# Kernel optimization log

Measured on AMD Instinct MI355X. Metric: run time of the kernel, lower is better.

The kernel has to match this reference:

```python
import jax, jax.numpy as jnp
import numpy as np

N_NODES = 100000
N_EDGES = 625000
IN_DIM = 128
NUM_CLASSES = 2


def setup_inputs() -> dict:
    key = jax.random.key(0)
    k1, k2, k3 = jax.random.split(key, 3)
    x = jax.random.normal(k1, (N_NODES, IN_DIM), dtype=jnp.float32)
    edge_index = jax.random.randint(k2, (2, N_EDGES), 0, N_NODES, dtype=jnp.int64)
    # nn.Linear(2*in_dim, num_classes): weight [out, in], bias [out]
    W = jax.random.normal(k3, (NUM_CLASSES, 2 * IN_DIM), dtype=jnp.float32) * (1.0 / np.sqrt(2 * IN_DIM))
    b = jnp.zeros((NUM_CLASSES,), dtype=jnp.float32)
    return {"x": x, "edge_index": edge_index, "W": W, "b": b}


def reference(x, edge_index, W, b):
    # Gather src/dst node features per edge, concat, linear classifier.
    src, dst = edge_index[0], edge_index[1]
    h = jnp.concatenate([x[src], x[dst]], axis=-1)  # [E, 2*in_dim]
    score = jnp.einsum('ed,cd->ec', h, W) + b        # [E, num_classes]
    return score
```

## Files before the change

### kernel.cpp

```cpp
#include <hip/hip_runtime.h>
#include <hip/hip_bf16.h>

#define IN_DIM 128

__global__ __launch_bounds__(256) void node_proj_kernel(
    const float* __restrict__ x,
    const float* __restrict__ W,
    float4* __restrict__ p,
    int n_nodes) {
    __shared__ __align__(16) float wlds[4 * 144];

    for (int i = threadIdx.x; i < 512; i += 256) {
        int c    = i >> 8;
        int d    = i & 255;
        int half = d >> 7;
        int k    = d & 127;
        int sub  = k >> 5;
        int kk   = k & 31;
        wlds[(half * 2 + c) * 144 + sub * 36 + kk] = W[i];
    }
    __syncthreads();

    const int lane = threadIdx.x & 63;
    const int sub  = lane & 3;
    const int nl   = lane >> 2;
    const int wave = threadIdx.x >> 6;
    const int node = (blockIdx.x * 4 + wave) * 16 + nl;

    if (node < n_nodes) {
        const float* xb = x + (size_t)node * IN_DIM + sub * 32;
        const float* wt = wlds + sub * 36;

        float a0 = 0.f, a1 = 0.f, d0 = 0.f, d1 = 0.f;
        #pragma unroll
        for (int j = 0; j < 8; ++j) {
            const float4 xv = *(const float4*)(xb + j * 4);
            const float4 w0 = *(const float4*)(wt + 0 * 144 + j * 4);
            const float4 w1 = *(const float4*)(wt + 1 * 144 + j * 4);
            const float4 w2 = *(const float4*)(wt + 2 * 144 + j * 4);
            const float4 w3 = *(const float4*)(wt + 3 * 144 + j * 4);
            a0 += xv.x * w0.x + xv.y * w0.y + xv.z * w0.z + xv.w * w0.w;
            a1 += xv.x * w1.x + xv.y * w1.y + xv.z * w1.z + xv.w * w1.w;
            d0 += xv.x * w2.x + xv.y * w2.y + xv.z * w2.z + xv.w * w2.w;
            d1 += xv.x * w3.x + xv.y * w3.y + xv.z * w3.z + xv.w * w3.w;
        }

        a0 += __shfl_xor(a0, 1, 64);
        a1 += __shfl_xor(a1, 1, 64);
        d0 += __shfl_xor(d0, 1, 64);
        d1 += __shfl_xor(d1, 1, 64);
        a0 += __shfl_xor(a0, 2, 64);
        a1 += __shfl_xor(a1, 2, 64);
        d0 += __shfl_xor(d0, 2, 64);
        d1 += __shfl_xor(d1, 2, 64);

        if (sub == 0) {
            p[node] = make_float4(a0, a1, d0, d1);
        }
    }
}

__global__ __launch_bounds__(256) void edge_score_kernel(
    const int* __restrict__ idx,
    const float4* __restrict__ p,
    const float* __restrict__ b,
    float2* __restrict__ out,
    int n_edges) {
    const int e = blockIdx.x * blockDim.x + threadIdx.x;
    if (e >= n_edges) return;
    const int s = idx[e];
    const int d = idx[n_edges + e];
    const float4 ps = p[s];
    const float4 pd = p[d];
    const float b0 = b[0];
    const float b1 = b[1];
    float2 o;
    o.x = ps.x + pd.z + b0;
    o.y = ps.y + pd.w + b1;
    out[e] = o;
}

extern "C" void kernel_launch(void* const* d_in, const int* in_sizes, int n_in,
                              void* d_out, int out_size, void* d_ws, size_t ws_size,
                              hipStream_t stream) {
    const float* x   = (const float*)d_in[0];
    const int*   idx = (const int*)d_in[1];
    const float* W   = (const float*)d_in[2];
    const float* b   = (const float*)d_in[3];
    float* out = (float*)d_out;

    const int n_nodes = in_sizes[0] / IN_DIM;
    const int n_edges = in_sizes[1] / 2;

    float4* p = (float4*)d_ws;

    const int blocks1 = (n_nodes + 63) / 64;
    node_proj_kernel<<<blocks1, 256, 0, stream>>>(x, W, p, n_nodes);

    const int blocks2 = (n_edges + 255) / 256;
    edge_score_kernel<<<blocks2, 256, 0, stream>>>(idx, p, b, (float2*)out, n_edges);
}
```

Measured before the change: 101.2 us.

## Fuse node projection and edge scoring into one persistent kernel with grid barrier

Merges the node-projection and edge-scoring kernels into a single persistent kernel of 256 blocks. Blocks synchronise through an atomic-counter grid barrier instead of a second launch. Edge indices are prefetched into registers before the projection phase so their load overlaps the node work. The projections are split into separate src/dst float2 arrays so each edge gather reads 8 bytes per endpoint instead of 16, and edges are handled four at a time with vectorised index loads and output stores. In exchange it adds a memset launch and a spin barrier that assumes all 256 blocks are co-resident, and it uses a fixed grid that may underfill the GPU.

```diff
diff --git a/kernel.cpp b/kernel.cpp
--- a/kernel.cpp
+++ b/kernel.cpp
@@ -2,15 +2,23 @@
 #include <hip/hip_bf16.h>
 
 #define IN_DIM 128
+#define NBLK 256
+#define NTHR 256
+#define MAX_GRP 3
 
-__global__ __launch_bounds__(256) void node_proj_kernel(
+__global__ __launch_bounds__(NTHR, 2) void fused_predictor_kernel(
     const float* __restrict__ x,
+    const int*   __restrict__ idx,
     const float* __restrict__ W,
-    float4* __restrict__ p,
-    int n_nodes) {
+    const float* __restrict__ b,
+    float*       __restrict__ out,
+    float2*      __restrict__ pa,
+    float2*      __restrict__ pd,
+    unsigned int* __restrict__ counter,
+    int n_nodes, int n_edges) {
     __shared__ __align__(16) float wlds[4 * 144];
 
-    for (int i = threadIdx.x; i < 512; i += 256) {
+    for (int i = threadIdx.x; i < 512; i += NTHR) {
         int c    = i >> 8;
         int d    = i & 255;
         int half = d >> 7;
@@ -19,65 +27,104 @@
         int kk   = k & 31;
         wlds[(half * 2 + c) * 144 + sub * 36 + kk] = W[i];
     }
+
+    const int tglob    = blockIdx.x * NTHR + threadIdx.x;
+    const int n_groups = n_edges >> 2;
+    int4 sg[MAX_GRP], dg[MAX_GRP];
+    #pragma unroll
+    for (int i = 0; i < MAX_GRP; ++i) {
+        int g = tglob + i * (NBLK * NTHR);
+        if (g < n_groups) {
+            sg[i] = *(const int4*)(idx + 4 * g);
+            dg[i] = *(const int4*)(idx + n_edges + 4 * g);
+        }
+    }
+    const float b0 = b[0];
+    const float b1 = b[1];
     __syncthreads();
 
     const int lane = threadIdx.x & 63;
     const int sub  = lane & 3;
     const int nl   = lane >> 2;
     const int wave = threadIdx.x >> 6;
-    const int node = (blockIdx.x * 4 + wave) * 16 + nl;
+    const int gwave  = blockIdx.x * 4 + wave;
+    const int stride = NBLK * 4 * 16;
 
-    if (node < n_nodes) {
-        const float* xb = x + (size_t)node * IN_DIM + sub * 32;
-        const float* wt = wlds + sub * 36;
-
-        float a0 = 0.f, a1 = 0.f, d0 = 0.f, d1 = 0.f;
-        #pragma unroll
-        for (int j = 0; j < 8; ++j) {
-            const float4 xv = *(const float4*)(xb + j * 4);
-            const float4 w0 = *(const float4*)(wt + 0 * 144 + j * 4);
-            const float4 w1 = *(const float4*)(wt + 1 * 144 + j * 4);
-            const float4 w2 = *(const float4*)(wt + 2 * 144 + j * 4);
-            const float4 w3 = *(const float4*)(wt + 3 * 144 + j * 4);
-            a0 += xv.x * w0.x + xv.y * w0.y + xv.z * w0.z + xv.w * w0.w;
-            a1 += xv.x * w1.x + xv.y * w1.y + xv.z * w1.z + xv.w * w1.w;
-            d0 += xv.x * w2.x + xv.y * w2.y + xv.z * w2.z + xv.w * w2.w;
-            d1 += xv.x * w3.x + xv.y * w3.y + xv.z * w3.z + xv.w * w3.w;
-        }
-
-        a0 += __shfl_xor(a0, 1, 64);
-        a1 += __shfl_xor(a1, 1, 64);
-        d0 += __shfl_xor(d0, 1, 64);
-        d1 += __shfl_xor(d1, 1, 64);
-        a0 += __shfl_xor(a0, 2, 64);
-        a1 += __shfl_xor(a1, 2, 64);
-        d0 += __shfl_xor(d0, 2, 64);
-        d1 += __shfl_xor(d1, 2, 64);
-
-        if (sub == 0) {
-            p[node] = make_float4(a0, a1, d0, d1);
+    const float* wt = wlds + sub * 36;
+    for (int base = gwave * 16; base < n_nodes; base += stride) {
+        const int node = base + nl;
+        if (node < n_nodes) {
+            const float* xb = x + (size_t)node * IN_DIM + sub * 32;
+            float a0 = 0.f, a1 = 0.f, d0 = 0.f, d1 = 0.f;
+            #pragma unroll
+            for (int j = 0; j < 8; ++j) {
+                const float4 xv = *(const float4*)(xb + j * 4);
+                const float4 w0 = *(const float4*)(wt + 0 * 144 + j * 4);
+                const float4 w1 = *(const float4*)(wt + 1 * 144 + j * 4);
+                const float4 w2 = *(const float4*)(wt + 2 * 144 + j * 4);
+                const float4 w3 = *(const float4*)(wt + 3 * 144 + j * 4);
+                a0 += xv.x * w0.x + xv.y * w0.y + xv.z * w0.z + xv.w * w0.w;
+                a1 += xv.x * w1.x + xv.y * w1.y + xv.z * w1.z + xv.w * w1.w;
+                d0 += xv.x * w2.x + xv.y * w2.y + xv.z * w2.z + xv.w * w2.w;
+                d1 += xv.x * w3.x + xv.y * w3.y + xv.z * w3.z + xv.w * w3.w;
+            }
+            a0 += __shfl_xor(a0, 1, 64);
+            a1 += __shfl_xor(a1, 1, 64);
+            d0 += __shfl_xor(d0, 1, 64);
+            d1 += __shfl_xor(d1, 1, 64);
+            a0 += __shfl_xor(a0, 2, 64);
+            a1 += __shfl_xor(a1, 2, 64);
+            d0 += __shfl_xor(d0, 2, 64);
+            d1 += __shfl_xor(d1, 2, 64);
+            if (sub == 0) pa[node] = make_float2(a0, a1);
+            if (sub == 1) pd[node] = make_float2(d0, d1);
         }
     }
-}
 
-__global__ __launch_bounds__(256) void edge_score_kernel(
-    const int* __restrict__ idx,
-    const float4* __restrict__ p,
-    const float* __restrict__ b,
-    float2* __restrict__ out,
-    int n_edges) {
-    const int e = blockIdx.x * blockDim.x + threadIdx.x;
-    if (e >= n_edges) return;
-    const int s = idx[e];
-    const int d = idx[n_edges + e];
-    const float4 ps = p[s];
-    const float4 pd = p[d];
-    const float b0 = b[0];
-    const float b1 = b[1];
-    float2 o;
-    o.x = ps.x + pd.z + b0;
-    o.y = ps.y + pd.w + b1;
-    out[e] = o;
+    __syncthreads();
+    if (threadIdx.x == 0) {
+        __threadfence();
+        __hip_atomic_fetch_add(counter, 1u, __ATOMIC_RELEASE, __HIP_MEMORY_SCOPE_AGENT);
+        while (__hip_atomic_load(counter, __ATOMIC_RELAXED, __HIP_MEMORY_SCOPE_AGENT)
+               < (unsigned)NBLK) {
+            __builtin_amdgcn_s_sleep(8);
+        }
+        __threadfence();
+    }
+    __syncthreads();
+
+    #pragma unroll
+    for (int i = 0; i < MAX_GRP; ++i) {
+        int g = tglob + i * (NBLK * NTHR);
+        if (g < n_groups) {
+            const float2 a0 = pa[sg[i].x];
+            const float2 a1 = pa[sg[i].y];
+            const float2 a2 = pa[sg[i].z];
+            const float2 a3 = pa[sg[i].w];
+            const float2 q0 = pd[dg[i].x];
+            const float2 q1 = pd[dg[i].y];
+            const float2 q2 = pd[dg[i].z];
+            const float2 q3 = pd[dg[i].w];
+            float4 o01, o23;
+            o01.x = a0.x + q0.x + b0;
+            o01.y = a0.y + q0.y + b1;
+            o01.z = a1.x + q1.x + b0;
+            o01.w = a1.y + q1.y + b1;
+            o23.x = a2.x + q2.x + b0;
+            o23.y = a2.y + q2.y + b1;
+            o23.z = a3.x + q3.x + b0;
+            o23.w = a3.y + q3.y + b1;
+            *(float4*)(out + 8 * (size_t)g)     = o01;
+            *(float4*)(out + 8 * (size_t)g + 4) = o23;
+        }
+    }
+    if (blockIdx.x == 0 && threadIdx.x < (n_edges & 3)) {
+        int e = (n_groups << 2) + threadIdx.x;
+        const float2 ps = pa[idx[e]];
+        const float2 pq = pd[idx[n_edges + e]];
+        out[2 * (size_t)e + 0] = ps.x + pq.x + b0;
+        out[2 * (size_t)e + 1] = ps.y + pq.y + b1;
+    }
 }
 
 extern "C" void kernel_launch(void* const* d_in, const int* in_sizes, int n_in,
@@ -92,11 +139,11 @@
     const int n_nodes = in_sizes[0] / IN_DIM;
     const int n_edges = in_sizes[1] / 2;
 
-    float4* p = (float4*)d_ws;
+    unsigned int* counter = (unsigned int*)d_ws;
+    float2* pa = (float2*)((char*)d_ws + 128);
+    float2* pd = pa + n_nodes;
 
-    const int blocks1 = (n_nodes + 63) / 64;
-    node_proj_kernel<<<blocks1, 256, 0, stream>>>(x, W, p, n_nodes);
-
-    const int blocks2 = (n_edges + 255) / 256;
-    edge_score_kernel<<<blocks2, 256, 0, stream>>>(idx, p, b, (float2*)out, n_edges);
+    hipMemsetAsync(counter, 0, sizeof(unsigned int), stream);
+    fused_predictor_kernel<<<NBLK, NTHR, 0, stream>>>(
+        x, idx, W, b, out, pa, pd, counter, n_nodes, n_edges);
 }
```

Measured after the change: 131.7 us. +30.1%, slower.
